# Optimization experiments

Measured on AMD Instinct MI355X. Metric: run time of the kernel, lower is better.

## Reference

```python
import jax, jax.numpy as jnp
import numpy as np

N_NODES = 100000
N_EDGES = 1600000
N_GRAPHS = 2048
NF = 64            # n_filters
N_INTER = 2        # n_interactions
U_MAX = 5.0
STEP = 0.1
GAMMA = 10.0
NG = 51            # number of gaussian rbf centers: arange(0, 5.0+step, 0.1)
LOG2 = float(np.log(2.0))


def ssp(x):
    # shifted softplus (SSPlus)
    return jax.nn.softplus(x) - LOG2


def _lin(key, fan_in, shape):
    return (jax.random.normal(key, shape) / np.sqrt(fan_in)).astype(jnp.float32)


def setup_inputs() -> dict:
    key = jax.random.key(0)
    ks = jax.random.split(key, 40)
    inp = {}
    inp['pos'] = jax.random.normal(ks[0], (N_NODES, 3), dtype=jnp.float32)
    inp['edge_index'] = jax.random.randint(ks[1], (2, N_EDGES), 0, N_NODES)
    inp['z'] = jax.random.randint(ks[2], (N_NODES,), 0, 100)
    inp['batch'] = jnp.sort(jax.random.randint(ks[3], (N_NODES,), 0, N_GRAPHS))
    inp['solvent'] = jax.random.randint(ks[4], (N_GRAPHS,), 0, 4)
    # embeddings (padding_idx=0 for atomic-number embedding)
    inp['emb_z'] = jax.random.normal(ks[5], (100, NF), dtype=jnp.float32).at[0].set(0.0)
    inp['emb_solv'] = jax.random.normal(ks[6], (4, 64), dtype=jnp.float32)
    # mlp_solv: 64 -> 64 -> 32
    inp['solv_w1'] = _lin(ks[7], 64, (64, 64)); inp['solv_b1'] = jnp.zeros((64,), jnp.float32)
    inp['solv_w2'] = _lin(ks[8], 64, (64, 32)); inp['solv_b2'] = jnp.zeros((32,), jnp.float32)
    # per-interaction params stacked over N_INTER
    inp['lin1_w'] = _lin(ks[9], NF, (N_INTER, NF, NF)); inp['lin1_b'] = jnp.zeros((N_INTER, NF), jnp.float32)
    inp['mlp_w1'] = _lin(ks[10], NF, (N_INTER, NF, NF)); inp['mlp_b1'] = jnp.zeros((N_INTER, NF), jnp.float32)
    inp['mlp_w2'] = _lin(ks[11], NF, (N_INTER, NF, NF)); inp['mlp_b2'] = jnp.zeros((N_INTER, NF), jnp.float32)
    inp['filt_w1'] = _lin(ks[12], NG, (N_INTER, NG, NF)); inp['filt_b1'] = jnp.zeros((N_INTER, NF), jnp.float32)
    inp['filt_w2'] = _lin(ks[13], NF, (N_INTER, NF, NF)); inp['filt_b2'] = jnp.zeros((N_INTER, NF), jnp.float32)
    # post_mlp: 64 -> 64 -> 64
    inp['post_w1'] = _lin(ks[14], NF, (NF, NF)); inp['post_b1'] = jnp.zeros((NF,), jnp.float32)
    inp['post_w2'] = _lin(ks[15], NF, (NF, 64)); inp['post_b2'] = jnp.zeros((64,), jnp.float32)
    # post_mlp2: 96 -> 128 -> 32 -> 1
    inp['post2_w1'] = _lin(ks[16], 96, (96, 128)); inp['post2_b1'] = jnp.zeros((128,), jnp.float32)
    inp['post2_w2'] = _lin(ks[17], 128, (128, 32)); inp['post2_b2'] = jnp.zeros((32,), jnp.float32)
    inp['post2_w3'] = _lin(ks[18], 32, (32, 1)); inp['post2_b3'] = jnp.zeros((1,), jnp.float32)
    return inp


def reference(pos, edge_index, z, batch, solvent,
              emb_z, emb_solv, solv_w1, solv_b1, solv_w2, solv_b2,
              lin1_w, lin1_b, mlp_w1, mlp_b1, mlp_w2, mlp_b2,
              filt_w1, filt_b1, filt_w2, filt_b2,
              post_w1, post_b1, post_w2, post_b2,
              post2_w1, post2_b1, post2_w2, post2_b2, post2_w3, post2_b3):
    n_nodes = pos.shape[0]
    n_graphs = solvent.shape[0]
    src, tgt = edge_index[0], edge_index[1]

    # node / solvent embeddings
    x = emb_z[z]                                            # [N, NF]
    s = emb_solv[solvent]                                   # [G, 64]
    s = ssp(s @ solv_w1 + solv_b1) @ solv_w2 + solv_b2      # [G, 32]

    # gaussian rbf expansion of edge distances (computed once, reused per block)
    centers = jnp.arange(0.0, U_MAX + STEP / 2, STEP, dtype=jnp.float32)  # [NG]
    d = jnp.linalg.norm(pos[src] - pos[tgt], axis=-1)       # [E]
    rbf = jnp.exp(-GAMMA * (d[:, None] - centers) ** 2)     # [E, NG]

    for i in range(N_INTER):
        m = x @ lin1_w[i] + lin1_b[i]                       # [N, NF]
        # CFConv filter network on rbf
        W = ssp(rbf @ filt_w1[i] + filt_b1[i]) @ filt_w2[i] + filt_b2[i]  # [E, NF]
        msg = m[src] * W                                    # gather + modulate
        agg = jax.ops.segment_sum(msg, tgt, num_segments=n_nodes)        # scatter-sum
        v = ssp(agg @ mlp_w1[i] + mlp_b1[i]) @ mlp_w2[i] + mlp_b2[i]
        x = x + v                                           # residual

    h = ssp(x @ post_w1 + post_b1) @ post_w2 + post_b2      # [N, 64]
    # scatter-mean pooling over graphs
    counts = jax.ops.segment_sum(jnp.ones((n_nodes,), h.dtype), batch, num_segments=n_graphs)
    pooled = jax.ops.segment_sum(h, batch, num_segments=n_graphs) / jnp.maximum(counts, 1.0)[:, None]

    out = jnp.concatenate([pooled, s], axis=1)              # [G, 96]
    out = ssp(out @ post2_w1 + post2_b1)
    out = ssp(out @ post2_w2 + post2_b2)
    out = out @ post2_w3 + post2_b3                         # [G, 1]
    return out
```

## Files before the change

kernel.cpp:

```cpp
#include <hip/hip_runtime.h>
#include <hip/hip_bf16.h>
#include <hip/hip_fp16.h>

#define TABN   4096
#define ROWS   (TABN + 1)
#define DMAX   6.5f
#define DELTA  (DMAX / (float)TABN)
#define INVD   ((float)TABN / DMAX)
#define LOG2F_ 0.6931471805599453f
#define SBITS  9
#define TILE   2048

typedef _Float16 f16x8 __attribute__((ext_vector_type(8)));
typedef float    f32x4 __attribute__((ext_vector_type(4)));

__device__ __forceinline__ float ssp(float x) {
    return fmaxf(x, 0.f) + __logf(1.f + __expf(-fabsf(x))) - LOG2F_;
}

__global__ void ftab_kernel(const float* __restrict__ fw1, const float* __restrict__ fb1,
                            const float* __restrict__ fw2, const float* __restrict__ fb2,
                            float* __restrict__ ftab) {
    int t = blockIdx.x;
    int i = blockIdx.y;
    int j = threadIdx.x;
    float d = (float)t * DELTA;
    float acc = fb1[i * 64 + j];
    for (int k = 0; k < 51; ++k) {
        float u = d - 0.1f * (float)k;
        float r = __expf(-10.f * u * u);
        acc = fmaf(r, fw1[((size_t)i * 51 + k) * 64 + j], acc);
    }
    __shared__ float h[64];
    h[j] = ssp(acc);
    __syncthreads();
    float o = fb2[i * 64 + j];
    for (int k = 0; k < 64; ++k)
        o = fmaf(h[k], fw2[((size_t)i * 64 + k) * 64 + j], o);
    ftab[((size_t)i * ROWS + t) * 64 + j] = o;
}

__global__ void fpack_kernel(const float* __restrict__ ftab, __half2* __restrict__ fpair) {
    int t = blockIdx.x, i = blockIdx.y, j = threadIdx.x;
    const float* r = ftab + ((size_t)i * ROWS + t) * 64;
    fpair[((size_t)i * TABN + t) * 64 + j] = __floats2half2_rn(r[j], r[j + 64]);
}

__global__ void wpack_kernel(const float* w0, const float* w1, const float* w2,
                             const float* w3, const float* w4, const float* w5,
                             const float* w6, __half* __restrict__ wt) {
    const float* ws[7] = {w0, w1, w2, w3, w4, w5, w6};
    int nrow = blockIdx.x, mat = blockIdx.y, k = threadIdx.x;
    wt[((size_t)mat * 64 + nrow) * 64 + k] = __float2half(ws[mat][k * 64 + nrow]);
}

__global__ void bhist_kernel(const int* __restrict__ ei, int* __restrict__ bcnt, int E) {
    __shared__ int h[256];
    int tid = threadIdx.x;
    h[tid] = 0;
    __syncthreads();
    for (int e = blockIdx.x * blockDim.x + tid; e < E; e += gridDim.x * blockDim.x)
        atomicAdd(&h[ei[E + e] >> SBITS], 1);
    __syncthreads();
    if (h[tid]) atomicAdd(&bcnt[tid], h[tid]);
}

__global__ void bscan_kernel(const int* __restrict__ bcnt, int* __restrict__ bbase,
                             int* __restrict__ bcur, int nbuck) {
    __shared__ int sm[256];
    int tid = threadIdx.x;
    int v = (tid < nbuck) ? bcnt[tid] : 0;
    sm[tid] = v;
    __syncthreads();
    for (int o = 1; o < 256; o <<= 1) {
        int t = (tid >= o) ? sm[tid - o] : 0;
        __syncthreads();
        sm[tid] += t;
        __syncthreads();
    }
    if (tid < nbuck) { bbase[tid] = sm[tid] - v; bcur[tid] = sm[tid] - v; }
    if (tid == 255) bbase[nbuck] = sm[255];
}

__global__ __launch_bounds__(256, 4)
void stage_kernel(const float* __restrict__ pos, const int* __restrict__ ei,
                  int* __restrict__ bcur, int2* __restrict__ stg, int E, int nbuck) {
    __shared__ int hist[256], loff[256], gbase[256], sc[256];
    __shared__ int2 sp[TILE];
    __shared__ short sb[TILE];
    int tid = threadIdx.x;
    int tile0 = blockIdx.x * TILE;
    int cnt = min(TILE, E - tile0);
    hist[tid] = 0;
    __syncthreads();
    int myrank[8], myb[8]; int2 mypay[8];
#pragma unroll
    for (int u = 0; u < 8; ++u) {
        int i = u * 256 + tid;
        myb[u] = -1;
        if (i < cnt) {
            int e = tile0 + i;
            int s = ei[e], t = ei[E + e];
            float dx = pos[3 * s]     - pos[3 * t];
            float dy = pos[3 * s + 1] - pos[3 * t + 1];
            float dz = pos[3 * s + 2] - pos[3 * t + 2];
            float d = sqrtf(dx * dx + dy * dy + dz * dz);
            float ds = fminf(d, DMAX) * INVD;
            int ti = min((int)ds, TABN - 1);
            int frq = min((int)((ds - (float)ti) * 1048576.f), 1048575);
            mypay[u] = make_int2(s | ((t & 511) << 17), (ti << 20) | frq);
            myb[u] = t >> SBITS;
            myrank[u] = atomicAdd(&hist[myb[u]], 1);
        }
    }
    __syncthreads();
    sc[tid] = hist[tid];
    __syncthreads();
    for (int o = 1; o < 256; o <<= 1) {
        int v = (tid >= o) ? sc[tid - o] : 0;
        __syncthreads();
        sc[tid] += v;
        __syncthreads();
    }
    loff[tid] = sc[tid] - hist[tid];
    if (tid < nbuck && hist[tid] > 0) gbase[tid] = atomicAdd(&bcur[tid], hist[tid]);
    __syncthreads();
#pragma unroll
    for (int u = 0; u < 8; ++u)
        if (myb[u] >= 0) {
            int idx = loff[myb[u]] + myrank[u];
            sp[idx] = mypay[u];
            sb[idx] = (short)myb[u];
        }
    __syncthreads();
    for (int i = tid; i < cnt; i += 256) {
        int b = sb[i];
        stg[gbase[b] + (i - loff[b])] = sp[i];
    }
}

__global__ __launch_bounds__(256)
void place_kernel(const int2* __restrict__ stg, const int* __restrict__ bbase,
                  int* __restrict__ off, int2* __restrict__ edata, int n, int nbuck) {
    int b = blockIdx.x;
    int n0 = b << SBITS;
    int nn = min(512, n - n0);
    int q0 = bbase[b], q1 = bbase[b + 1];
    __shared__ int cnt[512], cur[512], sc[256];
    int tid = threadIdx.x;
    cnt[tid] = 0; cnt[tid + 256] = 0;
    __syncthreads();
    for (int q = q0 + tid; q < q1; q += 256)
        atomicAdd(&cnt[(stg[q].x >> 17) & 511], 1);
    __syncthreads();
    int c0 = cnt[2 * tid], c1 = cnt[2 * tid + 1];
    int s = c0 + c1;
    sc[tid] = s;
    __syncthreads();
    for (int o = 1; o < 256; o <<= 1) {
        int v = (tid >= o) ? sc[tid - o] : 0;
        __syncthreads();
        sc[tid] += v;
        __syncthreads();
    }
    int run = sc[tid] - s;
    cur[2 * tid] = run;
    cur[2 * tid + 1] = run + c0;
    if (2 * tid < nn)     off[n0 + 2 * tid]     = q0 + run;
    if (2 * tid + 1 < nn) off[n0 + 2 * tid + 1] = q0 + run + c0;
    if (b == nbuck - 1 && tid == 0) off[n] = q1;
    __syncthreads();
    for (int q = q0 + tid; q < q1; q += 256) {
        int2 v = stg[q];
        int p = atomicAdd(&cur[(v.x >> 17) & 511], 1);
        edata[q0 + p] = v;
    }
}

__global__ void solv_kernel(const float* __restrict__ emb_solv,
                            const float* __restrict__ w1, const float* __restrict__ b1,
                            const float* __restrict__ w2, const float* __restrict__ b2,
                            float* __restrict__ s4) {
    __shared__ float h[4][64];
    int t = threadIdx.x, r = t >> 6, j = t & 63;
    float acc = b1[j];
    for (int k = 0; k < 64; ++k) acc = fmaf(emb_solv[r * 64 + k], w1[k * 64 + j], acc);
    h[r][j] = ssp(acc);
    __syncthreads();
    if (j < 32) {
        float a = b2[j];
        for (int k = 0; k < 64; ++k) a = fmaf(h[r][k], w2[k * 32 + j], a);
        s4[r * 32 + j] = a;
    }
}

__global__ __launch_bounds__(256, 4)
void mm1h_kernel(const int* __restrict__ z, const float* __restrict__ emb,
                 const float* __restrict__ w, const float* __restrict__ b,
                 __half* __restrict__ out, int n) {
    int tid = threadIdx.x;
    int q = __builtin_amdgcn_readfirstlane(tid >> 6);
    int node = blockIdx.x * 64 + (tid & 63);
    node = min(node, n - 1);
    int zi = z[node];
    const float4* in4 = (const float4*)(emb + (size_t)zi * 64);
    const float* wq = w + q * 16;
    const float* bq = b + q * 16;
    float acc[16];
#pragma unroll
    for (int j = 0; j < 16; ++j) acc[j] = bq[j];
#pragma unroll 2
    for (int kk = 0; kk < 16; ++kk) {
        float4 xv = in4[kk];
        const float* w0 = wq + kk * 256;
#pragma unroll
        for (int j = 0; j < 16; ++j) acc[j] = fmaf(xv.x, w0[j],       acc[j]);
#pragma unroll
        for (int j = 0; j < 16; ++j) acc[j] = fmaf(xv.y, w0[64 + j],  acc[j]);
#pragma unroll
        for (int j = 0; j < 16; ++j) acc[j] = fmaf(xv.z, w0[128 + j], acc[j]);
#pragma unroll
        for (int j = 0; j < 16; ++j) acc[j] = fmaf(xv.w, w0[192 + j], acc[j]);
    }
    __half2* o2 = (__half2*)(out + (size_t)node * 64 + q * 16);
#pragma unroll
    for (int c = 0; c < 8; ++c)
        o2[c] = __floats2half2_rn(acc[2 * c], acc[2 * c + 1]);
}

__global__ void agg_kernel(const int* __restrict__ off, const int2* __restrict__ edata,
                           const __half* __restrict__ m, const __half2* __restrict__ fpair,
                           __half* __restrict__ agg, int n) {
    int wave = (blockIdx.x * blockDim.x + threadIdx.x) >> 6;
    int lane = threadIdx.x & 63;
    if (wave >= n) return;
    int e0 = __builtin_amdgcn_readfirstlane(off[wave]);
    int e1 = __builtin_amdgcn_readfirstlane(off[wave + 1]);
    const float FRS = 1.f / 1048576.f;
    float acc[4] = {0.f, 0.f, 0.f, 0.f};
    int e = e0;
    for (; e + 8 <= e1; e += 8) {
        float mv[8], wv[8];
#pragma unroll
        for (int u = 0; u < 8; ++u) {
            int2 pd = edata[e + u];
            int px = __builtin_amdgcn_readfirstlane(pd.x);
            int py = __builtin_amdgcn_readfirstlane(pd.y);
            int s = px & 0x1FFFF;
            unsigned ti = ((unsigned)py) >> 20;
            float fr = (float)(py & 0xFFFFF) * FRS;
            mv[u] = __half2float(m[(size_t)s * 64 + lane]);
            float2 wf = __half22float2(fpair[(size_t)ti * 64 + lane]);
            wv[u] = fmaf(fr, wf.y - wf.x, wf.x);
        }
#pragma unroll
        for (int u = 0; u < 8; ++u) acc[u & 3] = fmaf(mv[u], wv[u], acc[u & 3]);
    }
    for (; e + 4 <= e1; e += 4) {
        float mv[4], wv[4];
#pragma unroll
        for (int u = 0; u < 4; ++u) {
            int2 pd = edata[e + u];
            int px = __builtin_amdgcn_readfirstlane(pd.x);
            int py = __builtin_amdgcn_readfirstlane(pd.y);
            int s = px & 0x1FFFF;
            unsigned ti = ((unsigned)py) >> 20;
            float fr = (float)(py & 0xFFFFF) * FRS;
            mv[u] = __half2float(m[(size_t)s * 64 + lane]);
            float2 wf = __half22float2(fpair[(size_t)ti * 64 + lane]);
            wv[u] = fmaf(fr, wf.y - wf.x, wf.x);
        }
#pragma unroll
        for (int u = 0; u < 4; ++u) acc[u] = fmaf(mv[u], wv[u], acc[u]);
    }
    for (; e < e1; ++e) {
        int2 pd = edata[e];
        int px = __builtin_amdgcn_readfirstlane(pd.x);
        int py = __builtin_amdgcn_readfirstlane(pd.y);
        int s = px & 0x1FFFF;
        unsigned ti = ((unsigned)py) >> 20;
        float fr = (float)(py & 0xFFFFF) * FRS;
        float mm = __half2float(m[(size_t)s * 64 + lane]);
        float2 wf = __half22float2(fpair[(size_t)ti * 64 + lane]);
        acc[0] = fmaf(mm, fmaf(fr, wf.y - wf.x, wf.x), acc[0]);
    }
    agg[(size_t)wave * 64 + lane] = __float2half((acc[0] + acc[1]) + (acc[2] + acc[3]));
}

template <int RESMODE, bool EMIT_M>
__global__ __launch_bounds__(256, 4)
void mfmlp_kernel(const __half* __restrict__ in,
                  const __half* __restrict__ w1t, const float* __restrict__ b1,
                  const __half* __restrict__ w2t, const float* __restrict__ b2,
                  const __half* __restrict__ res, const int* __restrict__ z,
                  const float* __restrict__ embf, __half* __restrict__ out,
                  const __half* __restrict__ lwt, const float* __restrict__ lb,
                  __half* __restrict__ mout, int n) {
    __shared__ __half hls[4][16][72];
    int tid = threadIdx.x;
    int w = tid >> 6, l = tid & 63;
    int lm = l & 15, lg = l >> 4;
    int base = blockIdx.x * 64 + w * 16;
    int arow = min(base + lm, n - 1);

    f32x4 acc[4];
#pragma unroll
    for (int nt = 0; nt < 4; ++nt) acc[nt] = (f32x4){0.f, 0.f, 0.f, 0.f};
#pragma unroll
    for (int s = 0; s < 2; ++s) {
        f16x8 a = *(const f16x8*)(in + (size_t)arow * 64 + 32 * s + 8 * lg);
#pragma unroll
        for (int nt = 0; nt < 4; ++nt) {
            f16x8 b = *(const f16x8*)(w1t + (size_t)(lm + 16 * nt) * 64 + 32 * s + 8 * lg);
            acc[nt] = __builtin_amdgcn_mfma_f32_16x16x32_f16(a, b, acc[nt], 0, 0, 0);
        }
    }
#pragma unroll
    for (int nt = 0; nt < 4; ++nt) {
        float bb = b1[lm + 16 * nt];
#pragma unroll
        for (int i = 0; i < 4; ++i)
            hls[w][lg * 4 + i][lm + 16 * nt] = __float2half(ssp(acc[nt][i] + bb));
    }

    f32x4 acc2[4];
#pragma unroll
    for (int nt = 0; nt < 4; ++nt) acc2[nt] = (f32x4){0.f, 0.f, 0.f, 0.f};
#pragma unroll
    for (int s = 0; s < 2; ++s) {
        f16x8 a = *(const f16x8*)(&hls[w][lm][32 * s + 8 * lg]);
#pragma unroll
        for (int nt = 0; nt < 4; ++nt) {
            f16x8 b = *(const f16x8*)(w2t + (size_t)(lm + 16 * nt) * 64 + 32 * s + 8 * lg);
            acc2[nt] = __builtin_amdgcn_mfma_f32_16x16x32_f16(a, b, acc2[nt], 0, 0, 0);
        }
    }
#pragma unroll
    for (int nt = 0; nt < 4; ++nt) {
        float bb = b2[lm + 16 * nt];
#pragma unroll
        for (int i = 0; i < 4; ++i) {
            int r = base + lg * 4 + i;
            if (r < n) {
                float v = acc2[nt][i] + bb;
                if constexpr (RESMODE == 1)
                    v += __half2float(res[(size_t)r * 64 + lm + 16 * nt]);
                else if constexpr (RESMODE == 2)
                    v += embf[(size_t)z[r] * 64 + lm + 16 * nt];
                out[(size_t)r * 64 + lm + 16 * nt] = __float2half(v);
                if constexpr (EMIT_M) hls[w][lg * 4 + i][lm + 16 * nt] = __float2half(v);
            }
        }
    }
    if constexpr (EMIT_M) {
        f32x4 acc3[4];
#pragma unroll
        for (int nt = 0; nt < 4; ++nt) acc3[nt] = (f32x4){0.f, 0.f, 0.f, 0.f};
#pragma unroll
        for (int s = 0; s < 2; ++s) {
            f16x8 a = *(const f16x8*)(&hls[w][lm][32 * s + 8 * lg]);
#pragma unroll
            for (int nt = 0; nt < 4; ++nt) {
                f16x8 b = *(const f16x8*)(lwt + (size_t)(lm + 16 * nt) * 64 + 32 * s + 8 * lg);
                acc3[nt] = __builtin_amdgcn_mfma_f32_16x16x32_f16(a, b, acc3[nt], 0, 0, 0);
            }
        }
#pragma unroll
        for (int nt = 0; nt < 4; ++nt) {
            float bb = lb[lm + 16 * nt];
#pragma unroll
            for (int i = 0; i < 4; ++i) {
                int r = base + lg * 4 + i;
                if (r < n)
                    mout[(size_t)r * 64 + lm + 16 * nt] = __float2half(acc3[nt][i] + bb);
            }
        }
    }
}

__global__ void pool_kernel(const __half* __restrict__ h, const int* __restrict__ batch,
                            float* __restrict__ pooled, int n_nodes) {
    int g = blockIdx.x, j = threadIdx.x;
    int lo = 0, hi = n_nodes;
    while (lo < hi) { int mid = (lo + hi) >> 1; if (batch[mid] < g) lo = mid + 1; else hi = mid; }
    int start = lo;
    int lo2 = start, hi2 = n_nodes;
    while (lo2 < hi2) { int mid = (lo2 + hi2) >> 1; if (batch[mid] < g + 1) lo2 = mid + 1; else hi2 = mid; }
    int end = lo2;
    float acc = 0.f;
    for (int r = start; r < end; ++r) acc += __half2float(h[(size_t)r * 64 + j]);
    float cnt = (float)(end - start);
    pooled[(size_t)g * 64 + j] = acc / fmaxf(cnt, 1.f);
}

__global__ void post2_kernel(const float* __restrict__ pooled, const float* __restrict__ s4,
                             const int* __restrict__ solvent,
                             const float* __restrict__ w1, const float* __restrict__ b1,
                             const float* __restrict__ w2, const float* __restrict__ b2,
                             const float* __restrict__ w3, const float* __restrict__ b3,
                             float* __restrict__ out) {
    __shared__ float in96[96];
    __shared__ float l1[128];
    __shared__ float l2[32];
    int g = blockIdx.x, t = threadIdx.x;
    if (t < 64)      in96[t] = pooled[(size_t)g * 64 + t];
    else if (t < 96) in96[t] = s4[solvent[g] * 32 + (t - 64)];
    __syncthreads();
    float acc = b1[t];
    for (int k = 0; k < 96; ++k) acc = fmaf(in96[k], w1[k * 128 + t], acc);
    l1[t] = ssp(acc);
    __syncthreads();
    if (t < 32) {
        float a = b2[t];
        for (int k = 0; k < 128; ++k) a = fmaf(l1[k], w2[k * 32 + t], a);
        l2[t] = ssp(a);
    }
    __syncthreads();
    if (t < 32) {
        float p = l2[t] * w3[t];
        for (int o = 16; o >= 1; o >>= 1) p += __shfl_down(p, o);
        if (t == 0) out[g] = p + b3[0];
    }
}

extern "C" void kernel_launch(void* const* d_in, const int* in_sizes, int n_in,
                              void* d_out, int out_size, void* d_ws, size_t ws_size,
                              hipStream_t stream) {
    const float* pos      = (const float*)d_in[0];
    const int*   ei       = (const int*)d_in[1];
    const int*   z        = (const int*)d_in[2];
    const int*   batch    = (const int*)d_in[3];
    const int*   solvent  = (const int*)d_in[4];
    const float* emb_z    = (const float*)d_in[5];
    const float* emb_solv = (const float*)d_in[6];
    const float* solv_w1  = (const float*)d_in[7];  const float* solv_b1 = (const float*)d_in[8];
    const float* solv_w2  = (const float*)d_in[9];  const float* solv_b2 = (const float*)d_in[10];
    const float* lin1_w   = (const float*)d_in[11]; const float* lin1_b  = (const float*)d_in[12];
    const float* mlp_w1   = (const float*)d_in[13]; const float* mlp_b1  = (const float*)d_in[14];
    const float* mlp_w2   = (const float*)d_in[15]; const float* mlp_b2  = (const float*)d_in[16];
    const float* filt_w1  = (const float*)d_in[17]; const float* filt_b1 = (const float*)d_in[18];
    const float* filt_w2  = (const float*)d_in[19]; const float* filt_b2 = (const float*)d_in[20];
    const float* post_w1  = (const float*)d_in[21]; const float* post_b1 = (const float*)d_in[22];
    const float* post_w2  = (const float*)d_in[23]; const float* post_b2 = (const float*)d_in[24];
    const float* p2w1 = (const float*)d_in[25]; const float* p2b1 = (const float*)d_in[26];
    const float* p2w2 = (const float*)d_in[27]; const float* p2b2 = (const float*)d_in[28];
    const float* p2w3 = (const float*)d_in[29]; const float* p2b3 = (const float*)d_in[30];
    float* out = (float*)d_out;

    const int N = in_sizes[2];
    const int E = in_sizes[1] / 2;
    const int G = in_sizes[4];
    const int NBUCK = (N + (1 << SBITS) - 1) >> SBITS;

    char* wp = (char*)d_ws;
    auto alloc = [&](size_t bytes) -> void* {
        void* r = (void*)wp;
        wp += (bytes + 255) & ~(size_t)255;
        return r;
    };
    int2*    stg    = (int2*)   alloc((size_t)E * 8);
    int2*    edata  = (int2*)   alloc((size_t)E * 8);
    int*     bcnt   = (int*)    alloc(256 * 4);
    int*     bbase  = (int*)    alloc(257 * 4);
    int*     bcur   = (int*)    alloc(256 * 4);
    int*     off    = (int*)    alloc((size_t)(N + 1) * 4);
    float*   ftab   = (float*)  alloc((size_t)2 * ROWS * 64 * 4);
    __half2* fpair  = (__half2*)alloc((size_t)2 * TABN * 64 * 4);
    __half*  wt     = (__half*) alloc((size_t)7 * 4096 * 2);
    float*   s4     = (float*)  alloc(4 * 32 * 4);
    __half*  x_h    = (__half*) alloc((size_t)N * 64 * 2);
    __half*  m_h    = (__half*) alloc((size_t)N * 64 * 2);
    __half*  m_h2   = (__half*) alloc((size_t)N * 64 * 2);
    __half*  agg_h  = (__half*) alloc((size_t)N * 64 * 2);
    __half*  hbuf   = (__half*) alloc((size_t)N * 64 * 2);
    float*   pooled = (float*)  alloc((size_t)G * 64 * 4);
    (void)ws_size; (void)n_in; (void)out_size;

    hipMemsetAsync(bcnt, 0, 256 * 4, stream);

    ftab_kernel<<<dim3(ROWS, 2), 64, 0, stream>>>(filt_w1, filt_b1, filt_w2, filt_b2, ftab);
    fpack_kernel<<<dim3(TABN, 2), 64, 0, stream>>>(ftab, fpair);
    wpack_kernel<<<dim3(64, 7), 64, 0, stream>>>(mlp_w1, mlp_w2, mlp_w1 + 4096,
                                                 mlp_w2 + 4096, post_w1, post_w2,
                                                 lin1_w + 4096, wt);
    bhist_kernel<<<512, 256, 0, stream>>>(ei, bcnt, E);
    bscan_kernel<<<1, 256, 0, stream>>>(bcnt, bbase, bcur, NBUCK);
    stage_kernel<<<(E + TILE - 1) / TILE, 256, 0, stream>>>(pos, ei, bcur, stg, E, NBUCK);
    place_kernel<<<NBUCK, 256, 0, stream>>>(stg, bbase, off, edata, N, NBUCK);
    solv_kernel<<<1, 256, 0, stream>>>(emb_solv, solv_w1, solv_b1, solv_w2, solv_b2, s4);

    int mmg = (N + 63) / 64;
    mm1h_kernel<<<mmg, 256, 0, stream>>>(z, emb_z, lin1_w, lin1_b, m_h, N);
    agg_kernel<<<(N + 3) / 4, 256, 0, stream>>>(off, edata, m_h, fpair, agg_h, N);
    mfmlp_kernel<2, true><<<mmg, 256, 0, stream>>>(
        agg_h, wt, mlp_b1, wt + 4096, mlp_b2, nullptr, z, emb_z, x_h,
        wt + 6 * 4096, lin1_b + 64, m_h2, N);
    agg_kernel<<<(N + 3) / 4, 256, 0, stream>>>(off, edata, m_h2,
                                                fpair + (size_t)TABN * 64, agg_h, N);
    mfmlp_kernel<1, false><<<mmg, 256, 0, stream>>>(
        agg_h, wt + 2 * 4096, mlp_b1 + 64, wt + 3 * 4096, mlp_b2 + 64, x_h,
        nullptr, nullptr, x_h, nullptr, nullptr, nullptr, N);
    mfmlp_kernel<0, false><<<mmg, 256, 0, stream>>>(
        x_h, wt + 4 * 4096, post_b1, wt + 5 * 4096, post_b2, nullptr,
        nullptr, nullptr, hbuf, nullptr, nullptr, nullptr, N);

    pool_kernel<<<G, 64, 0, stream>>>(hbuf, batch, pooled, N);
    post2_kernel<<<G, 128, 0, stream>>>(pooled, s4, solvent, p2w1, p2b1, p2w2, p2b2,
                                        p2w3, p2b3, out);
}
```

Measured before the change: 329.6 us.

## Replace bucket histogram/scan with fixed-capacity buckets and fuse filter table packing

Measured after the change: 310.6 us. 1.06x faster.

```diff
diff --git a/kernel.cpp b/kernel.cpp
--- a/kernel.cpp
+++ b/kernel.cpp
@@ -18,9 +18,9 @@
     return fmaxf(x, 0.f) + __logf(1.f + __expf(-fabsf(x))) - LOG2F_;
 }
 
-__global__ void ftab_kernel(const float* __restrict__ fw1, const float* __restrict__ fb1,
-                            const float* __restrict__ fw2, const float* __restrict__ fb2,
-                            float* __restrict__ ftab) {
+__global__ void ftabh_kernel(const float* __restrict__ fw1, const float* __restrict__ fb1,
+                             const float* __restrict__ fw2, const float* __restrict__ fb2,
+                             __half* __restrict__ fpairh) {
     int t = blockIdx.x;
     int i = blockIdx.y;
     int j = threadIdx.x;
@@ -37,13 +37,9 @@
     float o = fb2[i * 64 + j];
     for (int k = 0; k < 64; ++k)
         o = fmaf(h[k], fw2[((size_t)i * 64 + k) * 64 + j], o);
-    ftab[((size_t)i * ROWS + t) * 64 + j] = o;
-}
-
-__global__ void fpack_kernel(const float* __restrict__ ftab, __half2* __restrict__ fpair) {
-    int t = blockIdx.x, i = blockIdx.y, j = threadIdx.x;
-    const float* r = ftab + ((size_t)i * ROWS + t) * 64;
-    fpair[((size_t)i * TABN + t) * 64 + j] = __floats2half2_rn(r[j], r[j + 64]);
+    __half hv = __float2half(o);
+    if (t < TABN) fpairh[(((size_t)i * TABN + t) * 64 + j) * 2] = hv;
+    if (t > 0)    fpairh[(((size_t)i * TABN + (t - 1)) * 64 + j) * 2 + 1] = hv;
 }
 
 __global__ void wpack_kernel(const float* w0, const float* w1, const float* w2,
@@ -54,37 +50,15 @@
     wt[((size_t)mat * 64 + nrow) * 64 + k] = __float2half(ws[mat][k * 64 + nrow]);
 }
 
-__global__ void bhist_kernel(const int* __restrict__ ei, int* __restrict__ bcnt, int E) {
-    __shared__ int h[256];
-    int tid = threadIdx.x;
-    h[tid] = 0;
-    __syncthreads();
-    for (int e = blockIdx.x * blockDim.x + tid; e < E; e += gridDim.x * blockDim.x)
-        atomicAdd(&h[ei[E + e] >> SBITS], 1);
-    __syncthreads();
-    if (h[tid]) atomicAdd(&bcnt[tid], h[tid]);
-}
-
-__global__ void bscan_kernel(const int* __restrict__ bcnt, int* __restrict__ bbase,
-                             int* __restrict__ bcur, int nbuck) {
-    __shared__ int sm[256];
-    int tid = threadIdx.x;
-    int v = (tid < nbuck) ? bcnt[tid] : 0;
-    sm[tid] = v;
-    __syncthreads();
-    for (int o = 1; o < 256; o <<= 1) {
-        int t = (tid >= o) ? sm[tid - o] : 0;
-        __syncthreads();
-        sm[tid] += t;
-        __syncthreads();
-    }
-    if (tid < nbuck) { bbase[tid] = sm[tid] - v; bcur[tid] = sm[tid] - v; }
-    if (tid == 255) bbase[nbuck] = sm[255];
+__global__ void binit_kernel(int* __restrict__ bcur, int nbuck, int cap) {
+    int b = blockIdx.x * blockDim.x + threadIdx.x;
+    if (b < nbuck) bcur[b] = b * cap;
 }
 
 __global__ __launch_bounds__(256, 4)
 void stage_kernel(const float* __restrict__ pos, const int* __restrict__ ei,
-                  int* __restrict__ bcur, int2* __restrict__ stg, int E, int nbuck) {
+                  int* __restrict__ bcur, int2* __restrict__ stg, int E, int nbuck,
+                  int cap) {
     __shared__ int hist[256], loff[256], gbase[256], sc[256];
     __shared__ int2 sp[TILE];
     __shared__ short sb[TILE];
@@ -135,17 +109,21 @@
     __syncthreads();
     for (int i = tid; i < cnt; i += 256) {
         int b = sb[i];
-        stg[gbase[b] + (i - loff[b])] = sp[i];
+        int idx = gbase[b] + (i - loff[b]);
+        if (idx < (b + 1) * cap)
+            stg[idx] = sp[i];
     }
 }
 
 __global__ __launch_bounds__(256)
-void place_kernel(const int2* __restrict__ stg, const int* __restrict__ bbase,
-                  int* __restrict__ off, int2* __restrict__ edata, int n, int nbuck) {
+void place_kernel(const int2* __restrict__ stg, const int* __restrict__ bcur,
+                  int* __restrict__ off, int* __restrict__ offE,
+                  int2* __restrict__ edata, int n, int nbuck, int cap) {
     int b = blockIdx.x;
     int n0 = b << SBITS;
     int nn = min(512, n - n0);
-    int q0 = bbase[b], q1 = bbase[b + 1];
+    int q0 = b * cap;
+    int q1 = min(bcur[b], q0 + cap);
     __shared__ int cnt[512], cur[512], sc[256];
     int tid = threadIdx.x;
     cnt[tid] = 0; cnt[tid + 256] = 0;
@@ -166,9 +144,14 @@
     int run = sc[tid] - s;
     cur[2 * tid] = run;
     cur[2 * tid + 1] = run + c0;
-    if (2 * tid < nn)     off[n0 + 2 * tid]     = q0 + run;
-    if (2 * tid + 1 < nn) off[n0 + 2 * tid + 1] = q0 + run + c0;
-    if (b == nbuck - 1 && tid == 0) off[n] = q1;
+    if (2 * tid < nn) {
+        off[n0 + 2 * tid]  = q0 + run;
+        offE[n0 + 2 * tid] = q0 + run + c0;
+    }
+    if (2 * tid + 1 < nn) {
+        off[n0 + 2 * tid + 1]  = q0 + run + c0;
+        offE[n0 + 2 * tid + 1] = q0 + run + c0 + c1;
+    }
     __syncthreads();
     for (int q = q0 + tid; q < q1; q += 256) {
         int2 v = stg[q];
@@ -228,14 +211,15 @@
         o2[c] = __floats2half2_rn(acc[2 * c], acc[2 * c + 1]);
 }
 
-__global__ void agg_kernel(const int* __restrict__ off, const int2* __restrict__ edata,
+__global__ void agg_kernel(const int* __restrict__ off, const int* __restrict__ offE,
+                           const int2* __restrict__ edata,
                            const __half* __restrict__ m, const __half2* __restrict__ fpair,
                            __half* __restrict__ agg, int n) {
     int wave = (blockIdx.x * blockDim.x + threadIdx.x) >> 6;
     int lane = threadIdx.x & 63;
     if (wave >= n) return;
     int e0 = __builtin_amdgcn_readfirstlane(off[wave]);
-    int e1 = __builtin_amdgcn_readfirstlane(off[wave + 1]);
+    int e1 = __builtin_amdgcn_readfirstlane(offE[wave]);
     const float FRS = 1.f / 1048576.f;
     float acc[4] = {0.f, 0.f, 0.f, 0.f};
     int e = e0;
@@ -451,6 +435,7 @@
     const int E = in_sizes[1] / 2;
     const int G = in_sizes[4];
     const int NBUCK = (N + (1 << SBITS) - 1) >> SBITS;
+    const int CAP = E / NBUCK + 1024;
 
     char* wp = (char*)d_ws;
     auto alloc = [&](size_t bytes) -> void* {
@@ -458,13 +443,11 @@
         wp += (bytes + 255) & ~(size_t)255;
         return r;
     };
-    int2*    stg    = (int2*)   alloc((size_t)E * 8);
-    int2*    edata  = (int2*)   alloc((size_t)E * 8);
-    int*     bcnt   = (int*)    alloc(256 * 4);
-    int*     bbase  = (int*)    alloc(257 * 4);
+    int2*    stg    = (int2*)   alloc((size_t)NBUCK * CAP * 8);
+    int2*    edata  = (int2*)   alloc((size_t)NBUCK * CAP * 8);
     int*     bcur   = (int*)    alloc(256 * 4);
-    int*     off    = (int*)    alloc((size_t)(N + 1) * 4);
-    float*   ftab   = (float*)  alloc((size_t)2 * ROWS * 64 * 4);
+    int*     off    = (int*)    alloc((size_t)N * 4);
+    int*     offE   = (int*)    alloc((size_t)N * 4);
     __half2* fpair  = (__half2*)alloc((size_t)2 * TABN * 64 * 4);
     __half*  wt     = (__half*) alloc((size_t)7 * 4096 * 2);
     float*   s4     = (float*)  alloc(4 * 32 * 4);
@@ -476,26 +459,24 @@
     float*   pooled = (float*)  alloc((size_t)G * 64 * 4);
     (void)ws_size; (void)n_in; (void)out_size;
 
-    hipMemsetAsync(bcnt, 0, 256 * 4, stream);
-
-    ftab_kernel<<<dim3(ROWS, 2), 64, 0, stream>>>(filt_w1, filt_b1, filt_w2, filt_b2, ftab);
-    fpack_kernel<<<dim3(TABN, 2), 64, 0, stream>>>(ftab, fpair);
+    binit_kernel<<<1, 256, 0, stream>>>(bcur, NBUCK, CAP);
+    ftabh_kernel<<<dim3(ROWS, 2), 64, 0, stream>>>(filt_w1, filt_b1, filt_w2, filt_b2,
+                                                   (__half*)fpair);
     wpack_kernel<<<dim3(64, 7), 64, 0, stream>>>(mlp_w1, mlp_w2, mlp_w1 + 4096,
                                                  mlp_w2 + 4096, post_w1, post_w2,
                                                  lin1_w + 4096, wt);
-    bhist_kernel<<<512, 256, 0, stream>>>(ei, bcnt, E);
-    bscan_kernel<<<1, 256, 0, stream>>>(bcnt, bbase, bcur, NBUCK);
-    stage_kernel<<<(E + TILE - 1) / TILE, 256, 0, stream>>>(pos, ei, bcur, stg, E, NBUCK);
-    place_kernel<<<NBUCK, 256, 0, stream>>>(stg, bbase, off, edata, N, NBUCK);
+    stage_kernel<<<(E + TILE - 1) / TILE, 256, 0, stream>>>(pos, ei, bcur, stg, E,
+                                                            NBUCK, CAP);
+    place_kernel<<<NBUCK, 256, 0, stream>>>(stg, bcur, off, offE, edata, N, NBUCK, CAP);
     solv_kernel<<<1, 256, 0, stream>>>(emb_solv, solv_w1, solv_b1, solv_w2, solv_b2, s4);
 
     int mmg = (N + 63) / 64;
     mm1h_kernel<<<mmg, 256, 0, stream>>>(z, emb_z, lin1_w, lin1_b, m_h, N);
-    agg_kernel<<<(N + 3) / 4, 256, 0, stream>>>(off, edata, m_h, fpair, agg_h, N);
+    agg_kernel<<<(N + 3) / 4, 256, 0, stream>>>(off, offE, edata, m_h, fpair, agg_h, N);
     mfmlp_kernel<2, true><<<mmg, 256, 0, stream>>>(
         agg_h, wt, mlp_b1, wt + 4096, mlp_b2, nullptr, z, emb_z, x_h,
         wt + 6 * 4096, lin1_b + 64, m_h2, N);
-    agg_kernel<<<(N + 3) / 4, 256, 0, stream>>>(off, edata, m_h2,
+    agg_kernel<<<(N + 3) / 4, 256, 0, stream>>>(off, offE, edata, m_h2,
                                                 fpair + (size_t)TABN * 64, agg_h, N);
     mfmlp_kernel<1, false><<<mmg, 256, 0, stream>>>(
         agg_h, wt + 2 * 4096, mlp_b1 + 64, wt + 3 * 4096, mlp_b2 + 64, x_h,
```
